# Kernel optimization log

Hardware: AMD Instinct MI355X
Metric: run time of the kernel (lower is better)

Reference implementation:

```python
import jax, jax.numpy as jnp
import numpy as np

C = 256
NUM_HEADS = 4
REDUCTION = 4
RED = C // REDUCTION           # 64
HEAD_DIM = RED // NUM_HEADS    # 16
SCALE = HEAD_DIM ** -0.5
LN_EPS = 1e-5


def setup_inputs() -> dict:
    key = jax.random.key(0)
    ks = jax.random.split(key, 9)
    B, H, W = 2, 64, 64
    x = jax.random.normal(ks[0], (B, C, H, W), dtype=jnp.float32)
    # LayerNorm params
    norm_w = jnp.ones((C,), jnp.float32)
    norm_b = jnp.zeros((C,), jnp.float32)
    # Linear weights (torch layout: [out, in]), y = x @ W.T
    qkv_w = jax.random.normal(ks[1], (3 * RED, C), jnp.float32) * (C ** -0.5)
    out_w = jax.random.normal(ks[2], (C, RED), jnp.float32) * (RED ** -0.5)
    # 1x1 conv weights, stored as [out_c, in_c]
    conv1_w = jax.random.normal(ks[3], (C // 2, C), jnp.float32) * (C ** -0.5)
    conv1_b = jax.random.normal(ks[4], (C // 2,), jnp.float32) * 0.01
    conv2_w = jax.random.normal(ks[5], (1, C // 2), jnp.float32) * ((C // 2) ** -0.5)
    conv2_b = jax.random.normal(ks[6], (1,), jnp.float32) * 0.01
    gamma = jnp.ones((1,), jnp.float32) * 0.5  # nonzero so output depends on attention
    return {"x": x, "norm_w": norm_w, "norm_b": norm_b, "qkv_w": qkv_w,
            "out_w": out_w, "conv1_w": conv1_w, "conv1_b": conv1_b,
            "conv2_w": conv2_w, "conv2_b": conv2_b, "gamma": gamma}


def reference(x, norm_w, norm_b, qkv_w, out_w, conv1_w, conv1_b, conv2_w, conv2_b, gamma):
    B, C_, H, W = x.shape
    N = H * W
    # [B, N, C]
    xf = x.reshape(B, C_, N).transpose(0, 2, 1)
    # LayerNorm over channel dim
    mu = jnp.mean(xf, axis=-1, keepdims=True)
    var = jnp.mean(jnp.square(xf - mu), axis=-1, keepdims=True)
    xn = (xf - mu) * jax.lax.rsqrt(var + LN_EPS) * norm_w + norm_b
    # QKV projection -> [B, N, 3*RED]
    qkv = jnp.einsum('bnc,oc->bno', xn, qkv_w)
    q, k, v = jnp.split(qkv, 3, axis=-1)
    def heads(t):  # [B, N, RED] -> [B, h, N, d]
        return t.reshape(B, N, NUM_HEADS, HEAD_DIM).transpose(0, 2, 1, 3)
    q, k, v = heads(q), heads(k), heads(v)
    attn = jax.nn.softmax(jnp.einsum('bhnd,bhmd->bhnm', q, k) * SCALE, axis=-1)
    # dynamic weight branch: two 1x1 convs on raw x
    d1 = jax.nn.relu(jnp.einsum('oc,bchw->bohw', conv1_w, x) + conv1_b[None, :, None, None])
    dyn = (jnp.einsum('oc,bchw->bohw', conv2_w, d1) + conv2_b[None, :, None, None])  # [B,1,H,W]
    dyn = dyn.reshape(B, 1, N)  # broadcast over heads
    # per-query row scaling of attention
    attn = attn * dyn[:, :, :, None]
    out = jnp.einsum('bhnm,bhmd->bhnd', attn, v)            # [B,h,N,d]
    out = out.transpose(0, 2, 1, 3).reshape(B, N, RED)      # [B,N,RED]
    out = jnp.einsum('bnr,cr->bnc', out, out_w)             # [B,N,C]
    out = out.transpose(0, 2, 1).reshape(B, C_, H, W)
    return jax.nn.sigmoid(gamma[0] * out + x)
```

## Files before the change

kernel.cpp:

```cpp
#include <hip/hip_runtime.h>
#include <cstdint>
#include <cstddef>

#define LOG2E 1.44269504088896340736f

typedef float  f32x16 __attribute__((ext_vector_type(16)));
typedef __bf16 bf16x8 __attribute__((ext_vector_type(8)));

union BF8 { bf16x8 v; uint u[4]; ushort us[8]; };

__device__ __forceinline__ uint pack_bf(float a, float b) {
    uint ua = __float_as_uint(a) + 0x8000u;
    uint ub = __float_as_uint(b) + 0x8000u;
    return __builtin_amdgcn_perm(ub, ua, 0x07060302u);
}
__device__ __forceinline__ float bf_lo(uint u) { return __uint_as_float(u << 16); }
__device__ __forceinline__ float bf_hi(uint u) { return __uint_as_float(u & 0xFFFF0000u); }

__global__ __launch_bounds__(256) void convert_w_kernel(
    const float* __restrict__ qkv_w, const float* __restrict__ c1w,
    const float* __restrict__ out_w,
    ushort* __restrict__ qkvw_b, ushort* __restrict__ c1w_b, ushort* __restrict__ ow_b)
{
    const int g = (blockIdx.x * 256 + threadIdx.x) * 4;
    const float* src; ushort* dst; int off; float sc = 1.f;
    if (g < 49152)      { src = qkv_w; dst = qkvw_b; off = g;
                          if (g < 16384) sc = 0.25f * LOG2E; }
    else if (g < 81920) { src = c1w;   dst = c1w_b;  off = g - 49152; }
    else                { src = out_w; dst = ow_b;   off = g - 81920; }
    float4 v = *(const float4*)(src + off);
    uint2 pk;
    pk.x = pack_bf(v.x * sc, v.y * sc);
    pk.y = pack_bf(v.z * sc, v.w * sc);
    *(uint2*)(dst + off) = pk;
}

__global__ __launch_bounds__(256) void lnqkv_kernel(
    const float* __restrict__ x, const float* __restrict__ nw, const float* __restrict__ nb,
    const ushort* __restrict__ qkvw_b, const ushort* __restrict__ c1w_b,
    const float* __restrict__ c1b, const float* __restrict__ c2w,
    const float* __restrict__ c2b,
    ushort* __restrict__ Qb, ushort* __restrict__ Kb, ushort* __restrict__ Vsw,
    float* __restrict__ dynb)
{
    __shared__ uint  XN[32 * 32 * 4];
    __shared__ uint  XR[32 * 32 * 4];
    __shared__ float trans[4][32 * 33];
    __shared__ float red1[256], red2[256];
    __shared__ float muS[32], rsS[32];

    const int t    = threadIdx.x;
    const int pg   = blockIdx.x;
    const int b    = pg >> 7;
    const int n0   = (pg & 127) * 32;

    {
        const int j  = t & 31;
        const int cg = t >> 5;
        const size_t xb = (size_t)b * 256 * 4096 + n0 + j;
        float v[32];
        #pragma unroll
        for (int i = 0; i < 32; ++i) v[i] = x[xb + (size_t)(cg * 32 + i) * 4096];
        float s1 = 0.f, s2 = 0.f;
        #pragma unroll
        for (int i = 0; i < 32; ++i) { s1 += v[i]; s2 += v[i] * v[i]; }
        #pragma unroll
        for (int kk = 0; kk < 4; ++kk) {
            uint4 pk;
            pk.x = pack_bf(v[kk * 8 + 0], v[kk * 8 + 1]);
            pk.y = pack_bf(v[kk * 8 + 2], v[kk * 8 + 3]);
            pk.z = pack_bf(v[kk * 8 + 4], v[kk * 8 + 5]);
            pk.w = pack_bf(v[kk * 8 + 6], v[kk * 8 + 7]);
            *(uint4*)&XR[((cg * 4 + kk) * 32 + j) * 4] = pk;
        }
        red1[t] = s1; red2[t] = s2;
        __syncthreads();
        if (t < 32) {
            float a = 0.f, q = 0.f;
            #pragma unroll
            for (int g2 = 0; g2 < 8; ++g2) { a += red1[g2 * 32 + t]; q += red2[g2 * 32 + t]; }
            float mu  = a * (1.f / 256.f);
            float var = q * (1.f / 256.f) - mu * mu;
            muS[t] = mu; rsS[t] = rsqrtf(fmaxf(var, 0.f) + 1e-5f);
        }
        __syncthreads();
        const float mu = muS[j], rs = rsS[j];
        #pragma unroll
        for (int kk = 0; kk < 4; ++kk) {
            const float4 w0 = *(const float4*)(nw + cg * 32 + kk * 8);
            const float4 w1 = *(const float4*)(nw + cg * 32 + kk * 8 + 4);
            const float4 b0 = *(const float4*)(nb + cg * 32 + kk * 8);
            const float4 b1 = *(const float4*)(nb + cg * 32 + kk * 8 + 4);
            float e0 = (v[kk * 8 + 0] - mu) * rs * w0.x + b0.x;
            float e1 = (v[kk * 8 + 1] - mu) * rs * w0.y + b0.y;
            float e2 = (v[kk * 8 + 2] - mu) * rs * w0.z + b0.z;
            float e3 = (v[kk * 8 + 3] - mu) * rs * w0.w + b0.w;
            float e4 = (v[kk * 8 + 4] - mu) * rs * w1.x + b1.x;
            float e5 = (v[kk * 8 + 5] - mu) * rs * w1.y + b1.y;
            float e6 = (v[kk * 8 + 6] - mu) * rs * w1.z + b1.z;
            float e7 = (v[kk * 8 + 7] - mu) * rs * w1.w + b1.w;
            uint4 o;
            o.x = pack_bf(e0, e1); o.y = pack_bf(e2, e3);
            o.z = pack_bf(e4, e5); o.w = pack_bf(e6, e7);
            *(uint4*)&XN[((cg * 4 + kk) * 32 + j) * 4] = o;
        }
    }
    __syncthreads();

    const int w    = t >> 6;
    const int lane = t & 63;
    const int m    = lane & 31;
    const int h    = lane >> 5;
    float* tr = trans[w];
    const ushort* xnB = (const ushort*)XN;
    const ushort* xrB = (const ushort*)XR;

    if (w < 3) {
        const ushort* ap0 = qkvw_b + ((size_t)(w * 64 + m)) * 256 + h * 8;
        const ushort* ap1 = ap0 + 32 * 256;
        f32x16 acc0, acc1;
        #pragma unroll
        for (int i = 0; i < 16; ++i) { acc0[i] = 0.f; acc1[i] = 0.f; }
        #pragma unroll 4
        for (int ks = 0; ks < 16; ++ks) {
            bf16x8 bf = *(const bf16x8*)(xnB + ((ks * 2 + h) * 32 + m) * 8);
            bf16x8 a0 = *(const bf16x8*)(ap0 + ks * 16);
            bf16x8 a1 = *(const bf16x8*)(ap1 + ks * 16);
            acc0 = __builtin_amdgcn_mfma_f32_32x32x16_bf16(a0, bf, acc0, 0, 0, 0);
            acc1 = __builtin_amdgcn_mfma_f32_32x32x16_bf16(a1, bf, acc1, 0, 0, 0);
        }
        for (int ti = 0; ti < 2; ++ti) {
            const f32x16& A = ti ? acc1 : acc0;
            #pragma unroll
            for (int r = 0; r < 16; ++r)
                tr[((r & 3) + 8 * (r >> 2) + 4 * h) * 33 + m] = A[r];
            if (w < 2) {
                ushort* dst = (w == 0) ? Qb : Kb;
                #pragma unroll
                for (int it = 0; it < 2; ++it) {
                    int unit = it * 2 + h;
                    int hl = unit >> 1, half = unit & 1;
                    float v0 = tr[(hl * 16 + half * 8 + 0) * 33 + m];
                    float v1 = tr[(hl * 16 + half * 8 + 1) * 33 + m];
                    float v2 = tr[(hl * 16 + half * 8 + 2) * 33 + m];
                    float v3 = tr[(hl * 16 + half * 8 + 3) * 33 + m];
                    float v4 = tr[(hl * 16 + half * 8 + 4) * 33 + m];
                    float v5 = tr[(hl * 16 + half * 8 + 5) * 33 + m];
                    float v6 = tr[(hl * 16 + half * 8 + 6) * 33 + m];
                    float v7 = tr[(hl * 16 + half * 8 + 7) * 33 + m];
                    uint4 pk;
                    pk.x = pack_bf(v0, v1); pk.y = pack_bf(v2, v3);
                    pk.z = pack_bf(v4, v5); pk.w = pack_bf(v6, v7);
                    int head = ti * 2 + hl;
                    *(uint4*)(dst + ((size_t)(b * 4 + head) * 4096 + n0 + m) * 16 + half * 8) = pk;
                }
            } else {
                int d = lane & 15, u = lane >> 4;
                #pragma unroll
                for (int it = 0; it < 4; ++it) {
                    int unit = it * 4 + u;
                    int hl = unit >> 3, sg = unit & 7;
                    float v0 = tr[(hl * 16 + d) * 33 + sg * 4 + 0];
                    float v1 = tr[(hl * 16 + d) * 33 + sg * 4 + 1];
                    float v2 = tr[(hl * 16 + d) * 33 + sg * 4 + 2];
                    float v3 = tr[(hl * 16 + d) * 33 + sg * 4 + 3];
                    uint2 pk; pk.x = pack_bf(v0, v1); pk.y = pack_bf(v2, v3);
                    int head = ti * 2 + hl;
                    *(uint2*)(Vsw + (((size_t)(b * 4 + head) * 1024 + (pg & 127) * 8 + sg) * 16 + d) * 4) = pk;
                }
            }
        }
    } else {
        f32x16 acc[4];
        #pragma unroll
        for (int ti = 0; ti < 4; ++ti)
            #pragma unroll
            for (int i = 0; i < 16; ++i) acc[ti][i] = 0.f;
        #pragma unroll 2
        for (int ks = 0; ks < 16; ++ks) {
            bf16x8 bf = *(const bf16x8*)(xrB + ((ks * 2 + h) * 32 + m) * 8);
            #pragma unroll
            for (int ti = 0; ti < 4; ++ti) {
                bf16x8 a = *(const bf16x8*)(c1w_b + ((size_t)(ti * 32 + m)) * 256 + ks * 16 + h * 8);
                acc[ti] = __builtin_amdgcn_mfma_f32_32x32x16_bf16(a, bf, acc[ti], 0, 0, 0);
            }
        }
        float partial = 0.f;
        for (int ti = 0; ti < 4; ++ti) {
            #pragma unroll
            for (int r = 0; r < 16; ++r)
                tr[((r & 3) + 8 * (r >> 2) + 4 * h) * 33 + m] = acc[ti][r];
            #pragma unroll
            for (int i = 0; i < 16; ++i) {
                int og = ti * 32 + h * 16 + i;
                partial += fmaxf(tr[(h * 16 + i) * 33 + m] + c1b[og], 0.f) * c2w[og];
            }
        }
        float tot = partial + __shfl_xor(partial, 32);
        if (lane < 32) dynb[(size_t)b * 4096 + n0 + m] = c2b[0] + tot;
    }
}

__global__ __launch_bounds__(256) void attn_kernel(
    const ushort* __restrict__ Qb, const ushort* __restrict__ Kb,
    const ushort* __restrict__ Vsw, float* __restrict__ AO2)
{
    const int t   = threadIdx.x;
    const int lid = t & 63;
    const int w   = t >> 6;
    const int c   = lid & 31;
    const int h   = lid >> 5;

    const int bi = blockIdx.x;
    const int kb = bi & 1;
    const int qb = (bi >> 1) & 31;
    const int bh = bi >> 6;
    const int nq = qb * 128 + w * 32;

    const bf16x8 qf = *(const bf16x8*)(Qb + ((size_t)bh * 4096 + nq + c) * 16 + h * 8);

    f32x16 oacc, zf;
    #pragma unroll
    for (int i = 0; i < 16; ++i) { oacc[i] = 0.f; zf[i] = 0.f; }

    const ushort* kp = Kb + ((size_t)bh * 4096 + kb * 2048 + c) * 16 + h * 8;
    const ushort* vb = Vsw + (size_t)bh * 65536 + ((size_t)kb * 512 + h) * 64 + c * 4;

    #pragma unroll 2
    for (int ch = 0; ch < 64; ++ch) {
        const bf16x8 kf = *(const bf16x8*)kp;
        f32x16 s = __builtin_amdgcn_mfma_f32_32x32x16_bf16(kf, qf, zf, 0, 0, 0);

        BF8 p1, p2;
        #pragma unroll
        for (int jj = 0; jj < 4; ++jj) {
            p1.u[jj] = pack_bf(__builtin_amdgcn_exp2f(s[2*jj]),   __builtin_amdgcn_exp2f(s[2*jj+1]));
            p2.u[jj] = pack_bf(__builtin_amdgcn_exp2f(s[8+2*jj]), __builtin_amdgcn_exp2f(s[8+2*jj+1]));
        }

        BF8 a1, a2;
        if (c < 16) {
            const uint2 g1 = *(const uint2*)(vb);
            const uint2 g2 = *(const uint2*)(vb + 128);
            const uint2 g3 = *(const uint2*)(vb + 256);
            const uint2 g4 = *(const uint2*)(vb + 384);
            a1.u[0] = g1.x; a1.u[1] = g1.y; a1.u[2] = g2.x; a1.u[3] = g2.y;
            a2.u[0] = g3.x; a2.u[1] = g3.y; a2.u[2] = g4.x; a2.u[3] = g4.y;
        } else {
            const uint f = (c == 16) ? 0x3F803F80u : 0u;
            a1.u[0] = a1.u[1] = a1.u[2] = a1.u[3] = f;
            a2.u[0] = a2.u[1] = a2.u[2] = a2.u[3] = f;
        }

        oacc = __builtin_amdgcn_mfma_f32_32x32x16_bf16(a1.v, p1.v, oacc, 0, 0, 0);
        oacc = __builtin_amdgcn_mfma_f32_32x32x16_bf16(a2.v, p2.v, oacc, 0, 0, 0);

        kp += 512; vb += 512;
    }

    float* ao = AO2 + ((size_t)(kb * 8 + bh) * 4096 + nq + c) * 20;
    float4 s0; s0.x = oacc[0]; s0.y = oacc[1]; s0.z = oacc[2]; s0.w = oacc[3];
    float4 s1; s1.x = oacc[4]; s1.y = oacc[5]; s1.z = oacc[6]; s1.w = oacc[7];
    *(float4*)(ao + 4 * h)     = s0;
    *(float4*)(ao + 8 + 4 * h) = s1;
    if (h == 0) ao[16] = oacc[8];
}

__global__ __launch_bounds__(256) void final_kernel(
    const float* __restrict__ AO2, const float* __restrict__ dynb,
    const ushort* __restrict__ ow_b, const float* __restrict__ x,
    const float* __restrict__ gamma, float* __restrict__ out)
{
    __shared__ float trans[4][32 * 33];
    const int t    = threadIdx.x;
    const int w    = t >> 6;
    const int lane = t & 63;
    const int m    = lane & 31;
    const int h    = lane >> 5;
    const int pg   = blockIdx.x;
    const int b    = pg >> 7;
    const int n0   = (pg & 127) * 32;
    float* tr = trans[w];

    const float dyn_px = dynb[(size_t)b * 4096 + n0 + m];
    const ushort* a0p = ow_b + ((size_t)(w * 64 + m)) * 64 + h * 8;
    const ushort* a1p = a0p + 32 * 64;

    f32x16 acc0, acc1;
    #pragma unroll
    for (int i = 0; i < 16; ++i) { acc0[i] = 0.f; acc1[i] = 0.f; }

    #pragma unroll
    for (int ks = 0; ks < 4; ++ks) {
        const float* r0 = AO2 + ((size_t)(b * 4 + ks) * 4096 + n0 + m) * 20;
        const float* r1 = r0 + (size_t)8 * 4096 * 20;
        float l   = r0[16] + r1[16];
        float fac = dyn_px / l;
        float4 u0 = *(const float4*)(r0 + h * 8);
        float4 u1 = *(const float4*)(r0 + h * 8 + 4);
        float4 t0 = *(const float4*)(r1 + h * 8);
        float4 t1 = *(const float4*)(r1 + h * 8 + 4);
        float e0 = (u0.x + t0.x) * fac, e1 = (u0.y + t0.y) * fac;
        float e2 = (u0.z + t0.z) * fac, e3 = (u0.w + t0.w) * fac;
        float e4 = (u1.x + t1.x) * fac, e5 = (u1.y + t1.y) * fac;
        float e6 = (u1.z + t1.z) * fac, e7 = (u1.w + t1.w) * fac;
        BF8 bfr;
        bfr.u[0] = pack_bf(e0, e1); bfr.u[1] = pack_bf(e2, e3);
        bfr.u[2] = pack_bf(e4, e5); bfr.u[3] = pack_bf(e6, e7);
        bf16x8 af0 = *(const bf16x8*)(a0p + ks * 16);
        bf16x8 af1 = *(const bf16x8*)(a1p + ks * 16);
        acc0 = __builtin_amdgcn_mfma_f32_32x32x16_bf16(af0, bfr.v, acc0, 0, 0, 0);
        acc1 = __builtin_amdgcn_mfma_f32_32x32x16_bf16(af1, bfr.v, acc1, 0, 0, 0);
    }

    const float g = gamma[0];
    for (int ti = 0; ti < 2; ++ti) {
        const f32x16& A = ti ? acc1 : acc0;
        #pragma unroll
        for (int r = 0; r < 16; ++r)
            tr[((r & 3) + 8 * (r >> 2) + 4 * h) * 33 + m] = A[r];
        int ob = w * 64 + ti * 32;
        #pragma unroll 4
        for (int it = 0; it < 16; ++it) {
            int o = it * 2 + h;
            float vv = tr[o * 33 + m];
            size_t idx = ((size_t)b * 256 + ob + o) * 4096 + n0 + m;
            float z = g * vv + x[idx];
            out[idx] = 1.f / (1.f + __builtin_amdgcn_exp2f(-z * LOG2E));
        }
    }
}

extern "C" void kernel_launch(void* const* d_in, const int* in_sizes, int n_in,
                              void* d_out, int out_size, void* d_ws, size_t ws_size,
                              hipStream_t stream)
{
    const float* x      = (const float*)d_in[0];
    const float* norm_w = (const float*)d_in[1];
    const float* norm_b = (const float*)d_in[2];
    const float* qkv_w  = (const float*)d_in[3];
    const float* out_w  = (const float*)d_in[4];
    const float* c1w    = (const float*)d_in[5];
    const float* c1b    = (const float*)d_in[6];
    const float* c2w    = (const float*)d_in[7];
    const float* c2b    = (const float*)d_in[8];
    const float* gamma  = (const float*)d_in[9];

    char* ws = (char*)d_ws;
    ushort* Qb     = (ushort*)ws;
    ushort* Kb     = Qb + 524288;
    ushort* Vsw    = Kb + 524288;
    ushort* qkvw_b = Vsw + 524288;
    ushort* c1w_b  = qkvw_b + 49152;
    ushort* ow_b   = c1w_b + 32768;
    float*  dynb   = (float*)(ws + 3342336);
    float*  AO2    = (float*)(ws + 3375104);

    hipLaunchKernelGGL(convert_w_kernel, dim3(96), dim3(256), 0, stream,
                       qkv_w, c1w, out_w, qkvw_b, c1w_b, ow_b);
    hipLaunchKernelGGL(lnqkv_kernel, dim3(256), dim3(256), 0, stream,
                       x, norm_w, norm_b, qkvw_b, c1w_b, c1b, c2w, c2b,
                       Qb, Kb, Vsw, dynb);
    hipLaunchKernelGGL(attn_kernel, dim3(512), dim3(256), 0, stream,
                       Qb, Kb, Vsw, AO2);
    hipLaunchKernelGGL(final_kernel, dim3(256), dim3(256), 0, stream,
                       AO2, dynb, ow_b, x, gamma, (float*)d_out);
}
```

Measured before the change: 133.7 us.

## Fuse attention and output projection kernels into one block per pixel group

Merges the attention kernel and the final projection/sigmoid kernel into a single 512-thread kernel where 8 waves (4 heads x 2 key halves) cover one 32-query tile. Partial outputs and row sums are combined through shared memory instead of a global AO2 buffer. This removes a global write/read round trip and one kernel launch. It adds a block barrier and more LDS per block, which may reduce occupancy.

```diff
diff --git a/kernel.cpp b/kernel.cpp
--- a/kernel.cpp
+++ b/kernel.cpp
@@ -201,23 +201,29 @@
     }
 }
 
-__global__ __launch_bounds__(256) void attn_kernel(
+__global__ __launch_bounds__(512) void attn_final_kernel(
     const ushort* __restrict__ Qb, const ushort* __restrict__ Kb,
-    const ushort* __restrict__ Vsw, float* __restrict__ AO2)
+    const ushort* __restrict__ Vsw, const float* __restrict__ dynb,
+    const ushort* __restrict__ ow_b, const float* __restrict__ x,
+    const float* __restrict__ gamma, float* __restrict__ out)
 {
-    const int t   = threadIdx.x;
-    const int lid = t & 63;
-    const int w   = t >> 6;
-    const int c   = lid & 31;
-    const int h   = lid >> 5;
-
-    const int bi = blockIdx.x;
-    const int kb = bi & 1;
-    const int qb = (bi >> 1) & 31;
-    const int bh = bi >> 6;
-    const int nq = qb * 128 + w * 32;
-
-    const bf16x8 qf = *(const bf16x8*)(Qb + ((size_t)bh * 4096 + nq + c) * 16 + h * 8);
+    __shared__ float OM[2][4][16][32];
+    __shared__ float LM[2][4][32];
+    __shared__ float trans[8][32 * 33];
+
+    const int t    = threadIdx.x;
+    const int w    = t >> 6;
+    const int lane = t & 63;
+    const int c    = lane & 31;
+    const int h    = lane >> 5;
+    const int hd   = w & 3;
+    const int kb   = w >> 2;
+    const int pg   = blockIdx.x;
+    const int b    = pg >> 7;
+    const int n0   = (pg & 127) * 32;
+    const int bh   = b * 4 + hd;
+
+    const bf16x8 qf = *(const bf16x8*)(Qb + ((size_t)bh * 4096 + n0 + c) * 16 + h * 8);
 
     f32x16 oacc, zf;
     #pragma unroll
@@ -258,76 +264,47 @@
         kp += 512; vb += 512;
     }
 
-    float* ao = AO2 + ((size_t)(kb * 8 + bh) * 4096 + nq + c) * 20;
-    float4 s0; s0.x = oacc[0]; s0.y = oacc[1]; s0.z = oacc[2]; s0.w = oacc[3];
-    float4 s1; s1.x = oacc[4]; s1.y = oacc[5]; s1.z = oacc[6]; s1.w = oacc[7];
-    *(float4*)(ao + 4 * h)     = s0;
-    *(float4*)(ao + 8 + 4 * h) = s1;
-    if (h == 0) ao[16] = oacc[8];
-}
-
-__global__ __launch_bounds__(256) void final_kernel(
-    const float* __restrict__ AO2, const float* __restrict__ dynb,
-    const ushort* __restrict__ ow_b, const float* __restrict__ x,
-    const float* __restrict__ gamma, float* __restrict__ out)
-{
-    __shared__ float trans[4][32 * 33];
-    const int t    = threadIdx.x;
-    const int w    = t >> 6;
-    const int lane = t & 63;
-    const int m    = lane & 31;
-    const int h    = lane >> 5;
-    const int pg   = blockIdx.x;
-    const int b    = pg >> 7;
-    const int n0   = (pg & 127) * 32;
+    #pragma unroll
+    for (int r = 0; r < 8; ++r)
+        OM[kb][hd][(r & 3) + 8 * (r >> 2) + 4 * h][c] = oacc[r];
+    if (h == 0) LM[kb][hd][c] = oacc[8];
+    __syncthreads();
+
+    const int m = c;
+    const float dyn_px = dynb[(size_t)b * 4096 + n0 + m];
+
+    f32x16 acc;
+    #pragma unroll
+    for (int i = 0; i < 16; ++i) acc[i] = 0.f;
+
+    #pragma unroll
+    for (int ks = 0; ks < 4; ++ks) {
+        float l   = LM[0][ks][m] + LM[1][ks][m];
+        float fac = dyn_px / l;
+        BF8 bfr;
+        #pragma unroll
+        for (int i = 0; i < 4; ++i) {
+            int d0 = h * 8 + 2 * i;
+            float e0 = (OM[0][ks][d0][m]     + OM[1][ks][d0][m])     * fac;
+            float e1 = (OM[0][ks][d0 + 1][m] + OM[1][ks][d0 + 1][m]) * fac;
+            bfr.u[i] = pack_bf(e0, e1);
+        }
+        bf16x8 af = *(const bf16x8*)(ow_b + (size_t)(w * 32 + m) * 64 + ks * 16 + h * 8);
+        acc = __builtin_amdgcn_mfma_f32_32x32x16_bf16(af, bfr.v, acc, 0, 0, 0);
+    }
+
     float* tr = trans[w];
-
-    const float dyn_px = dynb[(size_t)b * 4096 + n0 + m];
-    const ushort* a0p = ow_b + ((size_t)(w * 64 + m)) * 64 + h * 8;
-    const ushort* a1p = a0p + 32 * 64;
-
-    f32x16 acc0, acc1;
-    #pragma unroll
-    for (int i = 0; i < 16; ++i) { acc0[i] = 0.f; acc1[i] = 0.f; }
-
-    #pragma unroll
-    for (int ks = 0; ks < 4; ++ks) {
-        const float* r0 = AO2 + ((size_t)(b * 4 + ks) * 4096 + n0 + m) * 20;
-        const float* r1 = r0 + (size_t)8 * 4096 * 20;
-        float l   = r0[16] + r1[16];
-        float fac = dyn_px / l;
-        float4 u0 = *(const float4*)(r0 + h * 8);
-        float4 u1 = *(const float4*)(r0 + h * 8 + 4);
-        float4 t0 = *(const float4*)(r1 + h * 8);
-        float4 t1 = *(const float4*)(r1 + h * 8 + 4);
-        float e0 = (u0.x + t0.x) * fac, e1 = (u0.y + t0.y) * fac;
-        float e2 = (u0.z + t0.z) * fac, e3 = (u0.w + t0.w) * fac;
-        float e4 = (u1.x + t1.x) * fac, e5 = (u1.y + t1.y) * fac;
-        float e6 = (u1.z + t1.z) * fac, e7 = (u1.w + t1.w) * fac;
-        BF8 bfr;
-        bfr.u[0] = pack_bf(e0, e1); bfr.u[1] = pack_bf(e2, e3);
-        bfr.u[2] = pack_bf(e4, e5); bfr.u[3] = pack_bf(e6, e7);
-        bf16x8 af0 = *(const bf16x8*)(a0p + ks * 16);
-        bf16x8 af1 = *(const bf16x8*)(a1p + ks * 16);
-        acc0 = __builtin_amdgcn_mfma_f32_32x32x16_bf16(af0, bfr.v, acc0, 0, 0, 0);
-        acc1 = __builtin_amdgcn_mfma_f32_32x32x16_bf16(af1, bfr.v, acc1, 0, 0, 0);
-    }
-
     const float g = gamma[0];
-    for (int ti = 0; ti < 2; ++ti) {
-        const f32x16& A = ti ? acc1 : acc0;
-        #pragma unroll
-        for (int r = 0; r < 16; ++r)
-            tr[((r & 3) + 8 * (r >> 2) + 4 * h) * 33 + m] = A[r];
-        int ob = w * 64 + ti * 32;
-        #pragma unroll 4
-        for (int it = 0; it < 16; ++it) {
-            int o = it * 2 + h;
-            float vv = tr[o * 33 + m];
-            size_t idx = ((size_t)b * 256 + ob + o) * 4096 + n0 + m;
-            float z = g * vv + x[idx];
-            out[idx] = 1.f / (1.f + __builtin_amdgcn_exp2f(-z * LOG2E));
-        }
+    #pragma unroll
+    for (int r = 0; r < 16; ++r)
+        tr[((r & 3) + 8 * (r >> 2) + 4 * h) * 33 + m] = acc[r];
+    #pragma unroll 4
+    for (int it = 0; it < 16; ++it) {
+        int o = it * 2 + h;
+        float vv = tr[o * 33 + m];
+        size_t idx = ((size_t)b * 256 + w * 32 + o) * 4096 + n0 + m;
+        float z = g * vv + x[idx];
+        out[idx] = 1.f / (1.f + __builtin_amdgcn_exp2f(-z * LOG2E));
     }
 }
 
@@ -354,15 +331,12 @@
     ushort* c1w_b  = qkvw_b + 49152;
     ushort* ow_b   = c1w_b + 32768;
     float*  dynb   = (float*)(ws + 3342336);
-    float*  AO2    = (float*)(ws + 3375104);
 
     hipLaunchKernelGGL(convert_w_kernel, dim3(96), dim3(256), 0, stream,
                        qkv_w, c1w, out_w, qkvw_b, c1w_b, ow_b);
     hipLaunchKernelGGL(lnqkv_kernel, dim3(256), dim3(256), 0, stream,
                        x, norm_w, norm_b, qkvw_b, c1w_b, c1b, c2w, c2b,
                        Qb, Kb, Vsw, dynb);
-    hipLaunchKernelGGL(attn_kernel, dim3(512), dim3(256), 0, stream,
-                       Qb, Kb, Vsw, AO2);
-    hipLaunchKernelGGL(final_kernel, dim3(256), dim3(256), 0, stream,
-                       AO2, dynb, ow_b, x, gamma, (float*)d_out);
-}
+    hipLaunchKernelGGL(attn_final_kernel, dim3(256), dim3(512), 0, stream,
+                       Qb, Kb, Vsw, dynb, ow_b, x, gamma, (float*)d_out);
+}
```

After: 125.2 us. 1.07x faster.
